# Kernel optimization log

Hardware: AMD Instinct MI355X
Metric: run time of the kernel (lower is better)

The kernel has to match this reference:

```python
import jax, jax.numpy as jnp
import numpy as np

B, S, D_IN, D_OUT, H = 4, 2048, 768, 768, 12
DH = D_OUT // H


def setup_inputs() -> dict:
    key = jax.random.key(0)
    ks = jax.random.split(key, 6)
    x = jax.random.normal(ks[0], (B, S, D_IN), dtype=jnp.float32)
    # causal mask: True above the diagonal means "masked out" (filled with -inf)
    mask = jnp.triu(jnp.ones((S, S), dtype=bool), k=1)
    sc = 1.0 / np.sqrt(D_IN)
    Wq = jax.random.normal(ks[1], (D_IN, D_OUT), dtype=jnp.float32) * sc
    Wk = jax.random.normal(ks[2], (D_IN, D_OUT), dtype=jnp.float32) * sc
    Wv = jax.random.normal(ks[3], (D_IN, D_OUT), dtype=jnp.float32) * sc
    Wo = jax.random.normal(ks[4], (D_OUT, D_OUT), dtype=jnp.float32) * (1.0 / np.sqrt(D_OUT))
    bo = jnp.zeros((D_OUT,), dtype=jnp.float32)
    return {"input_tensor": x, "mask": mask, "Wq": Wq, "Wk": Wk, "Wv": Wv, "Wo": Wo, "bo": bo}


def reference(input_tensor, mask, Wq, Wk, Wv, Wo, bo):
    b, n, _ = input_tensor.shape
    # projections -> [b, h, n, dh]
    q = (input_tensor @ Wq).reshape(b, n, H, DH).transpose(0, 2, 1, 3)
    k = (input_tensor @ Wk).reshape(b, n, H, DH).transpose(0, 2, 1, 3)
    v = (input_tensor @ Wv).reshape(b, n, H, DH).transpose(0, 2, 1, 3)
    # scores [b, h, n, n]
    scores = jnp.einsum('bhqd,bhkd->bhqk', q, k)
    scores = jnp.where(mask[:n, :n], -jnp.inf, scores)
    attn = jax.nn.softmax(scores / np.sqrt(DH), axis=-1)
    ctx = jnp.einsum('bhqk,bhkd->bhqd', attn, v)
    ctx = ctx.transpose(0, 2, 1, 3).reshape(b, n, D_OUT)
    return ctx @ Wo + bo
```

## Files before the change

kernel.cpp:

```cpp
#include <hip/hip_runtime.h>
#include <hip/hip_bf16.h>
#include <math.h>

typedef __attribute__((ext_vector_type(4))) float f32x4;
typedef __attribute__((ext_vector_type(8))) short s16x8;
typedef __attribute__((ext_vector_type(8))) unsigned short u16x8;

#define B_ 4
#define S_ 2048
#define DIN 768
#define DOUT 768
#define H_ 12
#define DH_ 64
#define M_ (B_*S_)

__device__ __forceinline__ unsigned short f2bf(float f) {
  union { float f; unsigned u; } v; v.f = f;
  unsigned r = v.u + 0x7fffu + ((v.u >> 16) & 1u);
  return (unsigned short)(r >> 16);
}


__global__ __launch_bounds__(256) void cast_x(const float* __restrict__ X,
                                              unsigned short* __restrict__ Xb) {
  size_t i = ((size_t)blockIdx.x * 256 + threadIdx.x) * 8;
  float4 a = *(const float4*)&X[i];
  float4 b = *(const float4*)&X[i + 4];
  u16x8 v;
  v[0] = f2bf(a.x); v[1] = f2bf(a.y); v[2] = f2bf(a.z); v[3] = f2bf(a.w);
  v[4] = f2bf(b.x); v[5] = f2bf(b.y); v[6] = f2bf(b.z); v[7] = f2bf(b.w);
  *(u16x8*)&Xb[i] = v;
}

__global__ __launch_bounds__(256) void tcast_w(
    const float* __restrict__ W0, const float* __restrict__ W1,
    const float* __restrict__ W2, const float* __restrict__ W3,
    unsigned short* __restrict__ Wt) {
  __shared__ float t[32][33];
  const float* W = blockIdx.z == 0 ? W0 : blockIdx.z == 1 ? W1
                 : blockIdx.z == 2 ? W2 : W3;
  unsigned short* Out = Wt + (size_t)blockIdx.z * DOUT * DIN;
  const int n0 = blockIdx.x * 32, k0 = blockIdx.y * 32;
  const int tx = threadIdx.x & 31, ty = threadIdx.x >> 5;
#pragma unroll
  for (int i = 0; i < 32; i += 8)
    t[ty + i][tx] = W[(size_t)(k0 + ty + i) * DOUT + n0 + tx];
  __syncthreads();
#pragma unroll
  for (int i = 0; i < 32; i += 8)
    Out[(size_t)(n0 + ty + i) * DIN + k0 + tx] = f2bf(t[tx][ty + i]);
}


#define BKC 32

__device__ __forceinline__ void stage_tile(
    const unsigned short* __restrict__ g, int row0, int k0,
    unsigned short* lds, int tid)
{
#pragma unroll
  for (int it = 0; it < 2; ++it) {
    int s = it * 256 + tid;
    int row = s >> 2, sc = s & 3;
    int gc = sc ^ ((row >> 1) & 3);
    const unsigned short* gsrc = g + (size_t)(row0 + row) * 768 + k0 + gc * 8;
    unsigned short* dst = lds + (size_t)(it * 256 + (tid & ~63)) * 8;
    __builtin_amdgcn_global_load_lds(
        (const __attribute__((address_space(1))) void*)gsrc,
        (__attribute__((address_space(3))) void*)dst, 16, 0, 0);
  }
}

__device__ __forceinline__ void gemm_core(
    const unsigned short* __restrict__ A, const unsigned short* __restrict__ Bt,
    int m0, int n0, unsigned short* As, unsigned short* Bs,
    f32x4 acc[4][4], int tid)
{
  const int lane = tid & 63;
  const int col_l = lane & 15, quad = lane >> 4;
  const int w = tid >> 6;
  const int wm = (w & 1) * 64, wn = (w >> 1) * 64;
  for (int k0 = 0; k0 < 768; k0 += BKC) {
    __syncthreads();
    stage_tile(A, m0, k0, As, tid);
    stage_tile(Bt, n0, k0, Bs, tid);
    __syncthreads();
    s16x8 af[4], bf[4];
#pragma unroll
    for (int t = 0; t < 4; ++t) {
      int ar = wm + t * 16 + col_l;
      af[t] = *(const s16x8*)&As[ar * 32 + (quad ^ ((ar >> 1) & 3)) * 8];
      int br = wn + t * 16 + col_l;
      bf[t] = *(const s16x8*)&Bs[br * 32 + (quad ^ ((br >> 1) & 3)) * 8];
    }
#pragma unroll
    for (int mt = 0; mt < 4; ++mt)
#pragma unroll
      for (int nt = 0; nt < 4; ++nt)
        acc[mt][nt] = __builtin_amdgcn_mfma_f32_16x16x32_bf16(
            af[mt], bf[nt], acc[mt][nt], 0, 0, 0);
  }
}

__global__ __launch_bounds__(256) void proj_mfma(
    const unsigned short* __restrict__ Xb, const unsigned short* __restrict__ Wt,
    unsigned short* __restrict__ Qo, unsigned short* __restrict__ Ko,
    unsigned short* __restrict__ Vo)
{
  __shared__ unsigned short As[128 * 32];
  __shared__ unsigned short Bs[128 * 32];
  const int tid = threadIdx.x;
  const int m0 = blockIdx.y * 128, n0 = blockIdx.x * 128;
  const int z = blockIdx.z;
  const unsigned short* Bw = Wt + (size_t)z * DOUT * DIN;
  unsigned short* Out = z == 0 ? Qo : z == 1 ? Ko : Vo;
  const float scale = z == 0 ? 0.125f : 1.0f;

  f32x4 acc[4][4] = {};
  gemm_core(Xb, Bw, m0, n0, As, Bs, acc, tid);

  const int lane = tid & 63, w = tid >> 6;
  const int col_l = lane & 15, quad = lane >> 4;
  const int wm = (w & 1) * 64, wn = (w >> 1) * 64;
  if (z == 2) {
    const int mblk = m0 + wm;
    const int b = mblk >> 11, sblk = mblk & (S_ - 1);
#pragma unroll
    for (int mt = 0; mt < 4; ++mt) {
      const int slot = (mt >> 1) * 32 + quad * 8 + (mt & 1) * 4;
#pragma unroll
      for (int nt = 0; nt < 4; ++nt) {
        int n = n0 + wn + nt * 16 + col_l;
        int h = n >> 6, d = n & 63;
        ushort4 v;
        v.x = f2bf(acc[mt][nt][0]); v.y = f2bf(acc[mt][nt][1]);
        v.z = f2bf(acc[mt][nt][2]); v.w = f2bf(acc[mt][nt][3]);
        *(ushort4*)&Out[((size_t)(b * H_ + h) * DH_ + d) * S_ + sblk + slot] = v;
      }
    }
  } else {
#pragma unroll
    for (int mt = 0; mt < 4; ++mt)
#pragma unroll
      for (int nt = 0; nt < 4; ++nt) {
        int n = n0 + wn + nt * 16 + col_l;
        int h = n >> 6, d = n & 63;
#pragma unroll
        for (int r = 0; r < 4; ++r) {
          int m = m0 + wm + mt * 16 + quad * 4 + r;
          int b = m >> 11, s = m & (S_ - 1);
          Out[((size_t)(b * H_ + h) * S_ + s) * DH_ + d] = f2bf(acc[mt][nt][r] * scale);
        }
      }
  }
}

__global__ __launch_bounds__(256) void out_mfma(
    const unsigned short* __restrict__ Cb, const unsigned short* __restrict__ Wt,
    const float* __restrict__ bo, float* __restrict__ Out)
{
  __shared__ unsigned short As[128 * 32];
  __shared__ unsigned short Bs[128 * 32];
  const int tid = threadIdx.x;
  const int m0 = blockIdx.y * 128, n0 = blockIdx.x * 128;

  f32x4 acc[4][4] = {};
  gemm_core(Cb, Wt, m0, n0, As, Bs, acc, tid);

  const int lane = tid & 63, w = tid >> 6;
  const int col_l = lane & 15, quad = lane >> 4;
  const int wm = (w & 1) * 64, wn = (w >> 1) * 64;
#pragma unroll
  for (int mt = 0; mt < 4; ++mt)
#pragma unroll
    for (int nt = 0; nt < 4; ++nt) {
      int n = n0 + wn + nt * 16 + col_l;
      float bias = bo[n];
#pragma unroll
      for (int r = 0; r < 4; ++r) {
        int m = m0 + wm + mt * 16 + quad * 4 + r;
        Out[(size_t)m * DOUT + n] = acc[mt][nt][r] + bias;
      }
    }
}


#define KSTR 72

union PK { uint2 u2[2]; s16x8 v; };

#define MFMA_BF16 __builtin_amdgcn_mfma_f32_16x16x32_bf16

__device__ __forceinline__ void exppack(const f32x4 sc[4], PK& p0, PK& p1) {
#pragma unroll
  for (int nc = 0; nc < 4; ++nc) {
    float e0 = __expf(sc[nc][0] - 12.0f);
    float e1 = __expf(sc[nc][1] - 12.0f);
    float e2 = __expf(sc[nc][2] - 12.0f);
    float e3 = __expf(sc[nc][3] - 12.0f);
    union { __hip_bfloat162 v; unsigned u; } lo, hi;
    lo.v = __float22bfloat162_rn(make_float2(e0, e1));
    hi.v = __float22bfloat162_rn(make_float2(e2, e3));
    uint2 pw; pw.x = lo.u; pw.y = hi.u;
    if (nc < 2) p0.u2[nc] = pw; else p1.u2[nc - 2] = pw;
  }
}

__global__ __launch_bounds__(256, 3) void attn_mfma(
    const unsigned short* __restrict__ Q, const unsigned short* __restrict__ K,
    const unsigned short* __restrict__ Vt, unsigned short* __restrict__ CTX)
{
  __shared__ unsigned short Ks[2][64 * KSTR];
  __shared__ unsigned short Vs[2][64 * KSTR];

  const int tid = threadIdx.x;
  const int lane = tid & 63;
  const int w = tid >> 6;
  const int col_l = lane & 15;
  const int quad = lane >> 4;
  const int b = blockIdx.z, h = blockIdx.y;
  const int p = blockIdx.x;
  const int q0A = p << 6, q0B = (31 - p) << 6;
  const int ntiles = 32 - p;
  const size_t bh = (size_t)(b * H_ + h);
  const unsigned short* Qg = Q + bh * S_ * DH_;
  const unsigned short* Kg = K + bh * S_ * DH_;
  const unsigned short* Vg = Vt + bh * DH_ * S_;

  const int qwA = q0A + (w << 4), qwB = q0B + (w << 4);
  s16x8 aqA0 = *(const s16x8*)&Qg[(size_t)(qwA + col_l) * DH_ + quad * 8];
  s16x8 aqA1 = *(const s16x8*)&Qg[(size_t)(qwA + col_l) * DH_ + 32 + quad * 8];
  s16x8 aqB0 = *(const s16x8*)&Qg[(size_t)(qwB + col_l) * DH_ + quad * 8];
  s16x8 aqB1 = *(const s16x8*)&Qg[(size_t)(qwB + col_l) * DH_ + 32 + quad * 8];

  const int krow = lane;
  const int vrow = tid >> 3;
  const int vslot = tid & 7;

  s16x8 kp0 = *(const s16x8*)&Kg[(size_t)krow * DH_ + w * 8];
  s16x8 kp1 = *(const s16x8*)&Kg[(size_t)krow * DH_ + (w + 4) * 8];
  s16x8 vp0 = *(const s16x8*)&Vg[(size_t)vrow * S_ + vslot * 8];
  s16x8 vp1 = *(const s16x8*)&Vg[(size_t)(vrow + 32) * S_ + vslot * 8];

  f32x4 oA[4] = {}, oB[4] = {}, lA = {}, lB = {};
  s16x8 bones;
#pragma unroll
  for (int i = 0; i < 8; ++i) bones[i] = (short)0x3F80;

  const int qrel = (w << 4) + col_l;

  for (int t = 0; t < ntiles; ++t) {
    unsigned short* KsB = &Ks[t & 1][0];
    unsigned short* VsB = &Vs[t & 1][0];
    *(s16x8*)&KsB[krow * KSTR + w * 8] = kp0;
    *(s16x8*)&KsB[krow * KSTR + (w + 4) * 8] = kp1;
    *(s16x8*)&VsB[vrow * KSTR + vslot * 8] = vp0;
    *(s16x8*)&VsB[(vrow + 32) * KSTR + vslot * 8] = vp1;
    __syncthreads();
    {
      const int jn = (t + 1 < ntiles ? t + 1 : t) << 6;
      kp0 = *(const s16x8*)&Kg[(size_t)(jn + krow) * DH_ + w * 8];
      kp1 = *(const s16x8*)&Kg[(size_t)(jn + krow) * DH_ + (w + 4) * 8];
      vp0 = *(const s16x8*)&Vg[(size_t)vrow * S_ + jn + vslot * 8];
      vp1 = *(const s16x8*)&Vg[(size_t)(vrow + 32) * S_ + jn + vslot * 8];
    }
    const bool doA = (t <= p);

    f32x4 scA[4], scB[4];
#pragma unroll
    for (int nc = 0; nc < 4; ++nc) {
      s16x8 k0 = *(const s16x8*)&KsB[(nc * 16 + col_l) * KSTR + quad * 8];
      s16x8 k1 = *(const s16x8*)&KsB[(nc * 16 + col_l) * KSTR + 32 + quad * 8];
      f32x4 a = {};
      a = MFMA_BF16(k0, aqB0, a, 0, 0, 0);
      a = MFMA_BF16(k1, aqB1, a, 0, 0, 0);
      scB[nc] = a;
      if (doA) {
        f32x4 c = {};
        c = MFMA_BF16(k0, aqA0, c, 0, 0, 0);
        c = MFMA_BF16(k1, aqA1, c, 0, 0, 0);
        scA[nc] = c;
      }
    }
    if (t == p) {
#pragma unroll
      for (int nc = 0; nc < 4; ++nc)
#pragma unroll
        for (int r = 0; r < 4; ++r)
          if (nc * 16 + quad * 4 + r > qrel) scA[nc][r] = -INFINITY;
    }
    if (t == ntiles - 1) {
#pragma unroll
      for (int nc = 0; nc < 4; ++nc)
#pragma unroll
        for (int r = 0; r < 4; ++r)
          if (nc * 16 + quad * 4 + r > qrel) scB[nc][r] = -INFINITY;
    }

    PK pA0, pA1, pB0, pB1;
    if (doA) exppack(scA, pA0, pA1);
    exppack(scB, pB0, pB1);

#pragma unroll
    for (int dc = 0; dc < 4; ++dc) {
      s16x8 b0 = *(const s16x8*)&VsB[(dc * 16 + col_l) * KSTR + quad * 8];
      s16x8 b1 = *(const s16x8*)&VsB[(dc * 16 + col_l) * KSTR + 32 + quad * 8];
      oB[dc] = MFMA_BF16(pB0.v, b0, oB[dc], 0, 0, 0);
      oB[dc] = MFMA_BF16(pB1.v, b1, oB[dc], 0, 0, 0);
      if (doA) {
        oA[dc] = MFMA_BF16(pA0.v, b0, oA[dc], 0, 0, 0);
        oA[dc] = MFMA_BF16(pA1.v, b1, oA[dc], 0, 0, 0);
      }
    }
    lB = MFMA_BF16(pB0.v, bones, lB, 0, 0, 0);
    lB = MFMA_BF16(pB1.v, bones, lB, 0, 0, 0);
    if (doA) {
      lA = MFMA_BF16(pA0.v, bones, lA, 0, 0, 0);
      lA = MFMA_BF16(pA1.v, bones, lA, 0, 0, 0);
    }
  }

  float liA[4], liB[4];
#pragma unroll
  for (int r = 0; r < 4; ++r) {
    liA[r] = 1.0f / lA[r];
    liB[r] = 1.0f / lB[r];
  }
#pragma unroll
  for (int dc = 0; dc < 4; ++dc)
#pragma unroll
    for (int r = 0; r < 4; ++r) {
      CTX[((size_t)(b * S_ + qwA + quad * 4 + r)) * DOUT + h * DH_ + dc * 16 + col_l]
          = f2bf(oA[dc][r] * liA[r]);
      CTX[((size_t)(b * S_ + qwB + quad * 4 + r)) * DOUT + h * DH_ + dc * 16 + col_l]
          = f2bf(oB[dc][r] * liB[r]);
    }
}


extern "C" void kernel_launch(void* const* d_in, const int* in_sizes, int n_in,
                              void* d_out, int out_size, void* d_ws, size_t ws_size,
                              hipStream_t stream) {
  const float* X  = (const float*)d_in[0];
  const float* Wq = (const float*)d_in[2];
  const float* Wk = (const float*)d_in[3];
  const float* Wv = (const float*)d_in[4];
  const float* Wo = (const float*)d_in[5];
  const float* bo = (const float*)d_in[6];
  float* out = (float*)d_out;

  unsigned short* Xb = (unsigned short*)d_ws;
  unsigned short* Wt = Xb + (size_t)M_ * DIN;
  unsigned short* Qb = Wt + (size_t)4 * DOUT * DIN;
  unsigned short* Kb = Qb + (size_t)M_ * DOUT;
  unsigned short* Vb = Kb + (size_t)M_ * DOUT;
  unsigned short* Cb = Vb + (size_t)M_ * DOUT;

  cast_x<<<dim3((M_ * DIN) / (256 * 8)), 256, 0, stream>>>(X, Xb);
  tcast_w<<<dim3(DOUT / 32, DIN / 32, 4), 256, 0, stream>>>(Wq, Wk, Wv, Wo, Wt);
  proj_mfma<<<dim3(DOUT / 128, M_ / 128, 3), 256, 0, stream>>>(Xb, Wt, Qb, Kb, Vb);
  attn_mfma<<<dim3(16, H_, B_), 256, 0, stream>>>(Qb, Kb, Vb, Cb);
  out_mfma<<<dim3(DOUT / 128, M_ / 128), 256, 0, stream>>>(
      Cb, Wt + (size_t)3 * DOUT * DIN, bo, out);
}
```

Measured before the change: 221.4 us.

## Double-buffer GEMM LDS tiles with register prefetch of next K slice

Replaces the direct global-to-LDS loads in the shared GEMM core with a register-staged, double-buffered pipeline. The next K slice is loaded into registers while MFMAs run on the current LDS buffer, and one of the two barriers per iteration is removed. The aim is to hide global load latency in both the projection and output GEMMs. In exchange it doubles LDS use per block, adds VGPR pressure, and writes LDS through registers instead of the direct async path.

```diff
diff --git a/kernel.cpp b/kernel.cpp
--- a/kernel.cpp
+++ b/kernel.cpp
@@ -52,25 +52,6 @@
 }
 
 
-#define BKC 32
-
-__device__ __forceinline__ void stage_tile(
-    const unsigned short* __restrict__ g, int row0, int k0,
-    unsigned short* lds, int tid)
-{
-#pragma unroll
-  for (int it = 0; it < 2; ++it) {
-    int s = it * 256 + tid;
-    int row = s >> 2, sc = s & 3;
-    int gc = sc ^ ((row >> 1) & 3);
-    const unsigned short* gsrc = g + (size_t)(row0 + row) * 768 + k0 + gc * 8;
-    unsigned short* dst = lds + (size_t)(it * 256 + (tid & ~63)) * 8;
-    __builtin_amdgcn_global_load_lds(
-        (const __attribute__((address_space(1))) void*)gsrc,
-        (__attribute__((address_space(3))) void*)dst, 16, 0, 0);
-  }
-}
-
 __device__ __forceinline__ void gemm_core(
     const unsigned short* __restrict__ A, const unsigned short* __restrict__ Bt,
     int m0, int n0, unsigned short* As, unsigned short* Bs,
@@ -80,18 +61,43 @@
   const int col_l = lane & 15, quad = lane >> 4;
   const int w = tid >> 6;
   const int wm = (w & 1) * 64, wn = (w >> 1) * 64;
-  for (int k0 = 0; k0 < 768; k0 += BKC) {
+
+  const int r0 = tid >> 2, sc = tid & 3;
+  const int r1 = (256 + tid) >> 2;
+  const int g0 = sc ^ ((r0 >> 1) & 3);
+  const int g1 = sc ^ ((r1 >> 1) & 3);
+  const unsigned short* a0p = A  + (size_t)(m0 + r0) * 768 + g0 * 8;
+  const unsigned short* a1p = A  + (size_t)(m0 + r1) * 768 + g1 * 8;
+  const unsigned short* b0p = Bt + (size_t)(n0 + r0) * 768 + g0 * 8;
+  const unsigned short* b1p = Bt + (size_t)(n0 + r1) * 768 + g1 * 8;
+
+  s16x8 pa0 = *(const s16x8*)a0p;
+  s16x8 pa1 = *(const s16x8*)a1p;
+  s16x8 pb0 = *(const s16x8*)b0p;
+  s16x8 pb1 = *(const s16x8*)b1p;
+
+  for (int k0 = 0; k0 < 768; k0 += 32) {
+    unsigned short* Ab = As + ((k0 >> 5) & 1) * (128 * 32);
+    unsigned short* Bb = Bs + ((k0 >> 5) & 1) * (128 * 32);
+    *(s16x8*)&Ab[(size_t)tid * 8] = pa0;
+    *(s16x8*)&Ab[(size_t)(256 + tid) * 8] = pa1;
+    *(s16x8*)&Bb[(size_t)tid * 8] = pb0;
+    *(s16x8*)&Bb[(size_t)(256 + tid) * 8] = pb1;
     __syncthreads();
-    stage_tile(A, m0, k0, As, tid);
-    stage_tile(Bt, n0, k0, Bs, tid);
-    __syncthreads();
+    {
+      const int kn = (k0 + 32 < 768) ? k0 + 32 : k0;
+      pa0 = *(const s16x8*)(a0p + kn);
+      pa1 = *(const s16x8*)(a1p + kn);
+      pb0 = *(const s16x8*)(b0p + kn);
+      pb1 = *(const s16x8*)(b1p + kn);
+    }
     s16x8 af[4], bf[4];
 #pragma unroll
     for (int t = 0; t < 4; ++t) {
       int ar = wm + t * 16 + col_l;
-      af[t] = *(const s16x8*)&As[ar * 32 + (quad ^ ((ar >> 1) & 3)) * 8];
+      af[t] = *(const s16x8*)&Ab[ar * 32 + (quad ^ ((ar >> 1) & 3)) * 8];
       int br = wn + t * 16 + col_l;
-      bf[t] = *(const s16x8*)&Bs[br * 32 + (quad ^ ((br >> 1) & 3)) * 8];
+      bf[t] = *(const s16x8*)&Bb[br * 32 + (quad ^ ((br >> 1) & 3)) * 8];
     }
 #pragma unroll
     for (int mt = 0; mt < 4; ++mt)
@@ -107,8 +113,8 @@
     unsigned short* __restrict__ Qo, unsigned short* __restrict__ Ko,
     unsigned short* __restrict__ Vo)
 {
-  __shared__ unsigned short As[128 * 32];
-  __shared__ unsigned short Bs[128 * 32];
+  __shared__ unsigned short As[2 * 128 * 32];
+  __shared__ unsigned short Bs[2 * 128 * 32];
   const int tid = threadIdx.x;
   const int m0 = blockIdx.y * 128, n0 = blockIdx.x * 128;
   const int z = blockIdx.z;
@@ -159,8 +165,8 @@
     const unsigned short* __restrict__ Cb, const unsigned short* __restrict__ Wt,
     const float* __restrict__ bo, float* __restrict__ Out)
 {
-  __shared__ unsigned short As[128 * 32];
-  __shared__ unsigned short Bs[128 * 32];
+  __shared__ unsigned short As[2 * 128 * 32];
+  __shared__ unsigned short Bs[2 * 128 * 32];
   const int tid = threadIdx.x;
   const int m0 = blockIdx.y * 128, n0 = blockIdx.x * 128;
 
```

Measured after the change: 223.7 us. Within noise of the previous version (+1.0%).
